# Performance work log

Hardware: AMD Instinct MI355X
Metric: run time of the kernel (lower is better)

The kernel has to match this reference:

```python
import jax, jax.numpy as jnp
import numpy as np

B, S, D, H = 2, 2048, 2048, 16
HD = D // H
EPS = 1e-5


def layernorm(x, scale, shift):
    mean = jnp.mean(x, axis=-1, keepdims=True)
    var = jnp.mean((x - mean) ** 2, axis=-1, keepdims=True)  # unbiased=False
    return scale * (x - mean) / jnp.sqrt(var + EPS) + shift


def gelu_buggy(x):
    # Faithful to source: tanh is applied ONLY to the constant sqrt(2/pi)
    c = jnp.tanh(jnp.sqrt(jnp.asarray(2.0 / jnp.pi, dtype=x.dtype)))
    return 0.5 * x * (1.0 + c * (x + 0.044715 * x ** 3))


def setup_inputs() -> dict:
    key = jax.random.key(0)
    ks = jax.random.split(key, 10)
    sd = 0.02
    return {
        "x": jax.random.normal(ks[0], (B, S, D), dtype=jnp.float32),
        "wq": jax.random.normal(ks[1], (D, D), dtype=jnp.float32) * sd,
        "wk": jax.random.normal(ks[2], (D, D), dtype=jnp.float32) * sd,
        "wv": jax.random.normal(ks[3], (D, D), dtype=jnp.float32) * sd,
        "wo": jax.random.normal(ks[4], (D, D), dtype=jnp.float32) * sd,
        "bo": jnp.zeros((D,), dtype=jnp.float32),
        "w1": jax.random.normal(ks[5], (D, 4 * D), dtype=jnp.float32) * sd,
        "b1": jnp.zeros((4 * D,), dtype=jnp.float32),
        "w2": jax.random.normal(ks[6], (4 * D, D), dtype=jnp.float32) * sd,
        "b2": jnp.zeros((D,), dtype=jnp.float32),
        "ln_scale": jnp.ones((D,), dtype=jnp.float32),
        "ln_shift": jnp.zeros((D,), dtype=jnp.float32),
    }


def attention(h, wq, wk, wv, wo, bo):
    b, s, _ = h.shape
    q = (h @ wq).reshape(b, s, H, HD).transpose(0, 2, 1, 3)  # [b,h,s,hd]
    k = (h @ wk).reshape(b, s, H, HD).transpose(0, 2, 1, 3)
    v = (h @ wv).reshape(b, s, H, HD).transpose(0, 2, 1, 3)
    scores = jnp.einsum('bhqd,bhkd->bhqk', q, k)
    causal = jnp.tril(jnp.ones((s, s), dtype=bool))
    scores = jnp.where(causal, scores, -jnp.inf)
    w = jax.nn.softmax(scores / jnp.sqrt(jnp.asarray(HD, dtype=h.dtype)), axis=-1)
    ctx = jnp.einsum('bhqk,bhkd->bhqd', w, v).transpose(0, 2, 1, 3).reshape(b, s, D)
    return ctx @ wo + bo


def reference(x, wq, wk, wv, wo, bo, w1, b1, w2, b2, ln_scale, ln_shift):
    # NB: source applies ln1 before BOTH sub-blocks (ln2 unused); dropout is identity (p=0 / eval)
    shortcut = x
    h = layernorm(x, ln_scale, ln_shift)
    h = attention(h, wq, wk, wv, wo, bo)
    x = h + shortcut
    shortcut = x
    h = layernorm(x, ln_scale, ln_shift)
    h = gelu_buggy(h @ w1 + b1) @ w2 + b2
    return h + shortcut
```

## Files before the change

kernel.cpp:

```cpp
#include <hip/hip_runtime.h>
#include <hip/hip_bf16.h>
#include <math.h>


typedef short bf16x8 __attribute__((ext_vector_type(8)));
typedef float f32x4 __attribute__((ext_vector_type(4)));
typedef short short4v __attribute__((ext_vector_type(4)));

#define MFMA16x32(a, b, c) __builtin_amdgcn_mfma_f32_16x16x32_bf16((a), (b), (c), 0, 0, 0)

__device__ __forceinline__ short f2bs(float f) {
    unsigned u = __builtin_bit_cast(unsigned, f);
    unsigned r = (u + 0x7FFFu + ((u >> 16) & 1u)) >> 16;
    return (short)(unsigned short)r;
}

__device__ __forceinline__ void gload_lds16(const void* g, void* l) {
    __builtin_amdgcn_global_load_lds(
        (const __attribute__((address_space(1))) unsigned int*)g,
        (__attribute__((address_space(3))) unsigned int*)l, 16, 0, 0);
}

template <int N>
__device__ __forceinline__ void vmw() {
    if constexpr (N == 0) asm volatile("s_waitcnt vmcnt(0)" ::: "memory");
    else if constexpr (N == 6) asm volatile("s_waitcnt vmcnt(6)" ::: "memory");
    else if constexpr (N == 8) asm volatile("s_waitcnt vmcnt(8)" ::: "memory");
    else if constexpr (N == 12) asm volatile("s_waitcnt vmcnt(12)" ::: "memory");
}

__global__ __launch_bounds__(256) void transpose_kernel(const float* __restrict__ in,
                                                        short* __restrict__ out,
                                                        int R, int C) {
    __shared__ float tile[32][33];
    const int tx = threadIdx.x & 31;
    const int ty = threadIdx.x >> 5;
    const int c0 = blockIdx.x * 32;
    const int r0 = blockIdx.y * 32;
#pragma unroll
    for (int i = 0; i < 4; ++i) {
        int r = ty + i * 8;
        tile[r][tx] = in[(size_t)(r0 + r) * C + c0 + tx];
    }
    __syncthreads();
#pragma unroll
    for (int i = 0; i < 4; ++i) {
        int r = ty + i * 8;
        out[(size_t)(c0 + r) * R + r0 + tx] = f2bs(tile[tx][r]);
    }
}

__global__ __launch_bounds__(256) void ln_kernel(const float* __restrict__ x,
                                                 const float* __restrict__ sc,
                                                 const float* __restrict__ sh,
                                                 short* __restrict__ out) {
    const int D = 2048;
    const int row = blockIdx.x;
    const int tid = threadIdx.x;
    __shared__ float red[4];
    const float4* xr = (const float4*)(x + (size_t)row * D);
    float4 v0 = xr[tid];
    float4 v1 = xr[tid + 256];
    float vals0[4] = {v0.x, v0.y, v0.z, v0.w};
    float vals1[4] = {v1.x, v1.y, v1.z, v1.w};

    float s = vals0[0] + vals0[1] + vals0[2] + vals0[3] + vals1[0] + vals1[1] + vals1[2] + vals1[3];
#pragma unroll
    for (int off = 32; off; off >>= 1) s += __shfl_xor(s, off);
    if ((tid & 63) == 0) red[tid >> 6] = s;
    __syncthreads();
    float mean = (red[0] + red[1] + red[2] + red[3]) * (1.0f / 2048.0f);
    __syncthreads();

    float q = 0.0f;
#pragma unroll
    for (int j = 0; j < 4; ++j) {
        float t0 = vals0[j] - mean;
        float t1 = vals1[j] - mean;
        q += t0 * t0 + t1 * t1;
    }
#pragma unroll
    for (int off = 32; off; off >>= 1) q += __shfl_xor(q, off);
    if ((tid & 63) == 0) red[tid >> 6] = q;
    __syncthreads();
    float var = (red[0] + red[1] + red[2] + red[3]) * (1.0f / 2048.0f);
    float inv = rsqrtf(var + 1e-5f);

    const int c0 = tid * 4;
    const int c1 = (tid + 256) * 4;
    short4v o0, o1;
#pragma unroll
    for (int j = 0; j < 4; ++j) {
        o0[j] = f2bs(sc[c0 + j] * ((vals0[j] - mean) * inv) + sh[c0 + j]);
        o1[j] = f2bs(sc[c1 + j] * ((vals1[j] - mean) * inv) + sh[c1 + j]);
    }
    *(short4v*)(out + (size_t)row * D + c0) = o0;
    *(short4v*)(out + (size_t)row * D + c1) = o1;
}

template <int EPI, int SK>
__global__ __launch_bounds__(512, 2) void gemm256(const short* __restrict__ Aop,
                                                  const short* __restrict__ Bt,
                                                  int M, int N, int K,
                                                  void* __restrict__ Cout,
                                                  float* __restrict__ part,
                                                  const float* __restrict__ bias,
                                                  const float* __restrict__ res,
                                                  float gconst) {
    constexpr int TSZ = 256 * 64;
    extern __shared__ __align__(16) short lds[];
    const int tid = threadIdx.x;
    const int lane = tid & 63;
    const int wid = tid >> 6;
    const int wm = wid >> 2, wn = wid & 3;
    const int l15 = lane & 15, grp = lane >> 4;

    const int gx = gridDim.x;
    int flat = (int)blockIdx.y * gx + (int)blockIdx.x;
    const int cpx = (gx * (int)gridDim.y) >> 3;
    flat = (flat & 7) * cpx + (flat >> 3);
    const int bx = flat % gx;
    const int byy = flat / gx;
    const int mtiles = M >> 8;
    const int myb = byy % mtiles;
    const int ksl = byy / mtiles;
    const long m0 = (long)myb * 256, n0 = (long)bx * 256;
    const int KS = K / SK;
    const long kbase = (long)ksl * KS;
    const int nt = KS >> 6;

    f32x4 zero = {0.f, 0.f, 0.f, 0.f};
    f32x4 acc[8][4];
#pragma unroll
    for (int i = 0; i < 8; i++)
#pragma unroll
        for (int j = 0; j < 4; j++) acc[i][j] = zero;

    auto STAGE = [&](int t, short* bufA, short* bufB) {
        const long k0 = kbase + ((long)t << 6);
#pragma unroll
        for (int j = 0; j < 4; ++j) {
            int c = tid + j * 512;
            int row = c >> 3, sl = (c & 7) ^ (row & 7);
            gload_lds16(Aop + (size_t)(m0 + row) * K + k0 + sl * 8, bufA + (size_t)c * 8);
        }
#pragma unroll
        for (int j = 0; j < 4; ++j) {
            int c = tid + j * 512;
            int row = c >> 3, sl = (c & 7) ^ (row & 7);
            gload_lds16(Bt + (size_t)(n0 + row) * K + k0 + sl * 8, bufB + (size_t)c * 8);
        }
    };

    STAGE(0, lds, lds + 2 * TSZ);
    STAGE(1, lds + TSZ, lds + 3 * TSZ);

    for (int t = 0; t < nt; ++t) {
        if (t == nt - 1) { vmw<0>(); } else { vmw<8>(); }
        __builtin_amdgcn_s_barrier();
        __builtin_amdgcn_sched_barrier(0);
        const short* bufA = lds + (t & 1) * TSZ;
        const short* bufB = lds + 2 * TSZ + (t & 1) * TSZ;
        __builtin_amdgcn_s_setprio(1);
#pragma unroll
        for (int kk = 0; kk < 2; ++kk) {
            bf16x8 af[8], bfr[4];
#pragma unroll
            for (int mi = 0; mi < 8; ++mi) {
                int row = wm * 128 + mi * 16 + l15;
                af[mi] = *(const bf16x8*)(bufA + row * 64 + (((kk * 4 + grp) ^ (row & 7)) * 8));
            }
#pragma unroll
            for (int ni = 0; ni < 4; ++ni) {
                int row = wn * 64 + ni * 16 + l15;
                bfr[ni] = *(const bf16x8*)(bufB + row * 64 + (((kk * 4 + grp) ^ (row & 7)) * 8));
            }
#pragma unroll
            for (int mi = 0; mi < 8; ++mi)
#pragma unroll
                for (int ni = 0; ni < 4; ++ni)
                    acc[mi][ni] = MFMA16x32(af[mi], bfr[ni], acc[mi][ni]);
        }
        __builtin_amdgcn_s_setprio(0);
        asm volatile("s_waitcnt lgkmcnt(0)" ::: "memory");
        __builtin_amdgcn_sched_barrier(0);
        __builtin_amdgcn_s_barrier();
        if (t + 2 < nt) STAGE(t + 2, lds + (t & 1) * TSZ, lds + 2 * TSZ + (t & 1) * TSZ);
    }

#pragma unroll
    for (int mi = 0; mi < 8; mi++) {
        long gr = m0 + wm * 128 + mi * 16 + grp * 4;
#pragma unroll
        for (int ni = 0; ni < 4; ni++) {
            long gcol = n0 + wn * 64 + ni * 16 + l15;
#pragma unroll
            for (int r = 0; r < 4; r++) {
                float vv = acc[mi][ni][r];
                long idx = (gr + r) * N + gcol;
                if constexpr (SK == 2) {
                    if (ksl == 1) part[idx] = vv;
                    else ((float*)Cout)[idx] = vv + bias[gcol] + res[idx];
                } else if constexpr (EPI == 0) {
                    ((short*)Cout)[idx] = f2bs(vv);
                } else {
                    float tv = vv + bias[gcol];
                    float g = 0.5f * tv * (1.0f + gconst * (tv + 0.044715f * tv * tv * tv));
                    ((short*)Cout)[idx] = f2bs(g);
                }
            }
        }
    }
}

template <int EPI>
__global__ __launch_bounds__(512, 1) void gemm3d(const short* __restrict__ A,
                                                 const short* __restrict__ Bt,
                                                 int M, int N, int K,
                                                 void* __restrict__ Cout,
                                                 const float* __restrict__ bias,
                                                 const float* __restrict__ res,
                                                 float gconst) {
    extern __shared__ __align__(16) short lds[];
    const int tid = threadIdx.x;
    const int lane = tid & 63;
    const int wid = tid >> 6;
    const int wm = wid >> 1, wn = wid & 1;
    const int l15 = lane & 15, grp = lane >> 4;

    const int gx = gridDim.x;
    int flat = (int)blockIdx.y * gx + (int)blockIdx.x;
    const int cpx = (gx * (int)gridDim.y) >> 3;
    flat = (flat & 7) * cpx + (flat >> 3);
    const int bx = flat % gx, by = flat / gx;
    const long m0 = (long)by * 256, n0 = (long)bx * 128;

    f32x4 zero = {0.f, 0.f, 0.f, 0.f};
    f32x4 acc[4][4];
#pragma unroll
    for (int i = 0; i < 4; i++)
#pragma unroll
        for (int j = 0; j < 4; j++) acc[i][j] = zero;

    auto STAGE = [&](long k0, int b) {
        short* bufA = lds + b * 24576;
        short* bufB = bufA + 16384;
#pragma unroll
        for (int j = 0; j < 4; ++j) {
            int c = tid + j * 512;
            int row = c >> 3, sl = (c & 7) ^ (row & 7);
            gload_lds16(A + (size_t)(m0 + row) * K + k0 + sl * 8,
                        bufA + (size_t)(wid * 64 + j * 512) * 8);
        }
#pragma unroll
        for (int j = 0; j < 2; ++j) {
            int c = tid + j * 512;
            int row = c >> 3, sl = (c & 7) ^ (row & 7);
            gload_lds16(Bt + (size_t)(n0 + row) * K + k0 + sl * 8,
                        bufB + (size_t)(wid * 64 + j * 512) * 8);
        }
    };

    const int nt = K >> 6;
    STAGE(0, 0);
    STAGE(64, 1);
    int cur = 0, nx2 = 2;

    for (int t = 0; t < nt; ++t) {
        if (t + 2 < nt) {
            STAGE((long)(t + 2) * 64, nx2);
            vmw<12>();
        } else if (t + 1 < nt) {
            vmw<6>();
        } else {
            vmw<0>();
        }
        __builtin_amdgcn_s_barrier();
        __builtin_amdgcn_sched_barrier(0);

        const short* bufA = lds + cur * 24576;
        const short* bufB = bufA + 16384;
        bf16x8 af[2][4], bfr[2][4];
#pragma unroll
        for (int kk = 0; kk < 2; ++kk) {
#pragma unroll
            for (int m = 0; m < 4; ++m) {
                int row = wm * 64 + m * 16 + l15;
                af[kk][m] = *(const bf16x8*)(bufA + row * 64 + (((kk * 4 + grp) ^ (row & 7)) * 8));
            }
#pragma unroll
            for (int n = 0; n < 4; ++n) {
                int row = wn * 64 + n * 16 + l15;
                bfr[kk][n] = *(const bf16x8*)(bufB + row * 64 + (((kk * 4 + grp) ^ (row & 7)) * 8));
            }
        }
        __builtin_amdgcn_s_setprio(1);
#pragma unroll
        for (int kk = 0; kk < 2; ++kk)
#pragma unroll
            for (int m = 0; m < 4; ++m)
#pragma unroll
                for (int n = 0; n < 4; ++n)
                    acc[m][n] = MFMA16x32(af[kk][m], bfr[kk][n], acc[m][n]);
        __builtin_amdgcn_s_setprio(0);
        asm volatile("s_waitcnt lgkmcnt(0)" ::: "memory");
        __builtin_amdgcn_s_barrier();
        __builtin_amdgcn_sched_barrier(0);
        cur = (cur == 2) ? 0 : cur + 1;
        nx2 = (nx2 == 2) ? 0 : nx2 + 1;
    }

#pragma unroll
    for (int m = 0; m < 4; m++) {
        long gr = m0 + wm * 64 + m * 16 + grp * 4;
#pragma unroll
        for (int n = 0; n < 4; n++) {
            long gcol = n0 + wn * 64 + n * 16 + l15;
#pragma unroll
            for (int r = 0; r < 4; r++) {
                float vv = acc[m][n][r];
                long idx = (gr + r) * N + gcol;
                if (EPI == 0) {
                    ((short*)Cout)[idx] = f2bs(vv);
                } else if (EPI == 1) {
                    ((float*)Cout)[idx] = vv + bias[gcol] + res[idx];
                } else {
                    float t2 = vv + bias[gcol];
                    float g = 0.5f * t2 * (1.0f + gconst * (t2 + 0.044715f * t2 * t2 * t2));
                    ((short*)Cout)[idx] = f2bs(g);
                }
            }
        }
    }
}

__global__ __launch_bounds__(256) void add_kernel(float* __restrict__ out,
                                                  const float* __restrict__ part,
                                                  int n4) {
    int i = blockIdx.x * 256 + threadIdx.x;
    int stride = gridDim.x * 256;
    for (; i < n4; i += stride) {
        float4 a = ((const float4*)out)[i];
        float4 b = ((const float4*)part)[i];
        a.x += b.x; a.y += b.y; a.z += b.z; a.w += b.w;
        ((float4*)out)[i] = a;
    }
}

__global__ __launch_bounds__(256) void reshape_k_kernel(const short* __restrict__ qkv,
                                                        short* __restrict__ Kh) {
    size_t idx = ((size_t)blockIdx.x * 256 + threadIdx.x) * 8;
    int d = (int)(idx & 127);
    int s = (int)((idx >> 7) & 2047);
    int bh = (int)(idx >> 18);
    int b = bh >> 4, h = bh & 15;
    const short* src = qkv + (size_t)(b * 2048 + s) * 6144 + 2048 + h * 128 + d;
    *(bf16x8*)(Kh + idx) = *(const bf16x8*)src;
}

__global__ __launch_bounds__(256) void reshape_v_kernel(const short* __restrict__ qkv,
                                                        short* __restrict__ Vt) {
    __shared__ short tile[32][33];
    const int bid = blockIdx.x;
    const int dt = bid & 3, st = (bid >> 2) & 63, bh = bid >> 8;
    const int b = bh >> 4, h = bh & 15;
    const int s0 = st * 32, d0 = dt * 32;
    const int tx = threadIdx.x & 31, ty = threadIdx.x >> 5;
#pragma unroll
    for (int i = 0; i < 4; ++i) {
        int s = ty + i * 8;
        tile[s][tx] = qkv[(size_t)(b * 2048 + s0 + s) * 6144 + 4096 + h * 128 + d0 + tx];
    }
    __syncthreads();
#pragma unroll
    for (int i = 0; i < 4; ++i) {
        int d = ty + i * 8;
        Vt[((size_t)bh * 128 + d0 + d) * 2048 + s0 + tx] = tile[tx][d];
    }
}

__global__ __launch_bounds__(256) void flash3_kernel(const short* __restrict__ qp,
                                                     const short* __restrict__ Kh,
                                                     const short* __restrict__ Vt,
                                                     short* __restrict__ ctx) {
    const int S = 2048, D = 2048, HD = 128, LD = 6144;
    __shared__ __align__(16) short Ks[2][64 * 128];
    __shared__ __align__(16) short Vs[2][64 * 128];
    __shared__ __align__(16) short Ps[4][16 * 64];
    const int tid = threadIdx.x;
    const int lane = tid & 63, wid = tid >> 6;
    const int l15 = lane & 15, grp = lane >> 4;

    int bid = (int)blockIdx.x;
    bid = (bid & 7) * 64 + (bid >> 3);
    const int p = bid & 15, bh = bid >> 4;
    const int b = bh >> 4, h = bh & 15;
    const int qtH = 31 - p;
    const int nH = qtH + 1;
    const float scale = 0.08838834764831845f;
    const float NEGINF = -__builtin_inff();

    const short* Kbase = Kh + (size_t)bh * S * 128;
    const short* Vbase = Vt + (size_t)bh * 128 * S;
    short* Psw = &Ps[wid][0];

    f32x4 zero = {0.f, 0.f, 0.f, 0.f};
    bf16x8 aq[4];
    float m_[4], l_[4];
    f32x4 o[8];

    int qt = qtH;
    int qw = qt * 64 + wid * 16;
    {
        const short* qrow = qp + (size_t)(b * S + qw + l15) * LD + h * HD;
#pragma unroll
        for (int kc = 0; kc < 4; kc++) aq[kc] = *(const bf16x8*)(qrow + kc * 32 + grp * 8);
    }
#pragma unroll
    for (int r = 0; r < 4; r++) { m_[r] = NEGINF; l_[r] = 0.f; }
#pragma unroll
    for (int n = 0; n < 8; n++) o[n] = zero;

#pragma unroll
    for (int j = 0; j < 4; ++j) {
        int c = tid + j * 256;
        int r = c >> 4, sl = c & 15;
        gload_lds16(Kbase + (size_t)r * 128 + ((sl ^ (r & 7)) * 8),
                    Ks[0] + (size_t)(wid * 64 + j * 256) * 8);
    }
#pragma unroll
    for (int j = 0; j < 4; ++j) {
        int c = tid + j * 256;
        int d = c >> 3, sl = c & 7;
        gload_lds16(Vbase + (size_t)d * S + ((sl ^ (d & 7)) * 8),
                    Vs[0] + (size_t)(wid * 64 + j * 256) * 8);
    }
    __syncthreads();

    int cur = 0;
    for (int i = 0; i < 33; ++i) {
        const int kt = (i < nH) ? i : (i - nH);
        const bool lastT = (kt == qt);

        if (i + 1 < 33) {
            const int ktn = (i + 1 < nH) ? (i + 1) : (i + 1 - nH);
            const long kn0 = (long)ktn * 64;
            const short* Kg = Kbase + kn0 * 128;
            const short* Vg = Vbase + kn0;
            short* kd = Ks[cur ^ 1];
            short* vd = Vs[cur ^ 1];
#pragma unroll
            for (int j = 0; j < 4; ++j) {
                int c = tid + j * 256;
                int r = c >> 4, sl = c & 15;
                gload_lds16(Kg + (size_t)r * 128 + ((sl ^ (r & 7)) * 8),
                            kd + (size_t)(wid * 64 + j * 256) * 8);
            }
#pragma unroll
            for (int j = 0; j < 4; ++j) {
                int c = tid + j * 256;
                int d = c >> 3, sl = c & 7;
                gload_lds16(Vg + (size_t)d * S + ((sl ^ (d & 7)) * 8),
                            vd + (size_t)(wid * 64 + j * 256) * 8);
            }
        }

        const short* Kc = Ks[cur];
        const short* Vc = Vs[cur];

        f32x4 s[4] = {zero, zero, zero, zero};
#pragma unroll
        for (int n = 0; n < 4; ++n) {
            int r = n * 16 + l15;
#pragma unroll
            for (int kc = 0; kc < 4; ++kc) {
                bf16x8 kb = *(const bf16x8*)(Kc + r * 128 + (((kc * 4 + grp) ^ (r & 7)) * 8));
                s[n] = MFMA16x32(aq[kc], kb, s[n]);
            }
        }

        float al[4];
#pragma unroll
        for (int r = 0; r < 4; ++r) {
            float v[4];
#pragma unroll
            for (int n = 0; n < 4; ++n) v[n] = s[n][r] * scale;
            if (lastT) {
                int qrel = wid * 16 + grp * 4 + r;
#pragma unroll
                for (int n = 0; n < 4; ++n)
                    if (n * 16 + l15 > qrel) v[n] = NEGINF;
            }
            float mx = fmaxf(fmaxf(v[0], v[1]), fmaxf(v[2], v[3]));
            mx = fmaxf(mx, __shfl_xor(mx, 1));
            mx = fmaxf(mx, __shfl_xor(mx, 2));
            mx = fmaxf(mx, __shfl_xor(mx, 4));
            mx = fmaxf(mx, __shfl_xor(mx, 8));
            float mn = fmaxf(m_[r], mx);
            float sc_ = __expf(m_[r] - mn);
            float rs = 0.f;
            int q = grp * 4 + r;
#pragma unroll
            for (int n = 0; n < 4; ++n) {
                v[n] = __expf(v[n] - mn);
                rs += v[n];
                Psw[q * 64 + (((n * 2 + (l15 >> 3)) ^ (q & 7)) * 8) + (l15 & 7)] = f2bs(v[n]);
            }
            rs += __shfl_xor(rs, 1);
            rs += __shfl_xor(rs, 2);
            rs += __shfl_xor(rs, 4);
            rs += __shfl_xor(rs, 8);
            l_[r] = l_[r] * sc_ + rs;
            m_[r] = mn;
            al[r] = sc_;
        }
#pragma unroll
        for (int n = 0; n < 8; n++) {
            f32x4 t = o[n];
            t[0] *= al[0]; t[1] *= al[1]; t[2] *= al[2]; t[3] *= al[3];
            o[n] = t;
        }

        bf16x8 pa[2];
#pragma unroll
        for (int kc = 0; kc < 2; ++kc)
            pa[kc] = *(const bf16x8*)(Psw + l15 * 64 + (((kc * 4 + grp) ^ (l15 & 7)) * 8));
#pragma unroll
        for (int n = 0; n < 8; ++n) {
            int d = n * 16 + l15;
#pragma unroll
            for (int kc = 0; kc < 2; ++kc) {
                bf16x8 vb = *(const bf16x8*)(Vc + d * 64 + (((kc * 4 + grp) ^ (d & 7)) * 8));
                o[n] = MFMA16x32(pa[kc], vb, o[n]);
            }
        }

        if (lastT) {
            float inv[4];
#pragma unroll
            for (int r = 0; r < 4; ++r) inv[r] = 1.0f / l_[r];
            short* cb_ = ctx + (size_t)(b * S + qw + grp * 4) * D + h * HD + l15;
#pragma unroll
            for (int n = 0; n < 8; ++n)
#pragma unroll
                for (int r = 0; r < 4; ++r)
                    cb_[(size_t)r * D + n * 16] = f2bs(o[n][r] * inv[r]);
            if (i < 32) {
                qt = 31 - qtH;
                qw = qt * 64 + wid * 16;
                const short* qrow = qp + (size_t)(b * S + qw + l15) * LD + h * HD;
#pragma unroll
                for (int kc = 0; kc < 4; kc++) aq[kc] = *(const bf16x8*)(qrow + kc * 32 + grp * 8);
#pragma unroll
                for (int r = 0; r < 4; r++) { m_[r] = NEGINF; l_[r] = 0.f; }
#pragma unroll
                for (int n = 0; n < 8; n++) o[n] = zero;
            }
        }
        __syncthreads();
        cur ^= 1;
    }
}

extern "C" void kernel_launch(void* const* d_in, const int* in_sizes, int n_in,
                              void* d_out, int out_size, void* d_ws, size_t ws_size,
                              hipStream_t stream) {
    const float* x    = (const float*)d_in[0];
    const float* wq   = (const float*)d_in[1];
    const float* wk   = (const float*)d_in[2];
    const float* wv   = (const float*)d_in[3];
    const float* wo   = (const float*)d_in[4];
    const float* bo   = (const float*)d_in[5];
    const float* w1   = (const float*)d_in[6];
    const float* b1   = (const float*)d_in[7];
    const float* w2   = (const float*)d_in[8];
    const float* b2   = (const float*)d_in[9];
    const float* lnsc = (const float*)d_in[10];
    const float* lnsh = (const float*)d_in[11];

    const int B = 2, S = 2048, D = 2048;
    const int M = B * S;
    const int LDS_256 = 4 * 256 * 64 * 2;
    const int LDS_3D  = 3 * 24576 * 2;

    char* p = (char*)d_ws;
    short* wqkvT = (short*)p; p += (size_t)3 * D * D * 2;
    short* woT   = (short*)p; p += (size_t)D * D * 2;
    short* w1T   = (short*)p; p += (size_t)4 * D * D * 2;
    short* w2T   = (short*)p; p += (size_t)4 * D * D * 2;
    short* lnb   = (short*)p; p += (size_t)M * D * 2;
    short* qkvb  = (short*)p;
    short* h1    = qkvb;
    p += (size_t)M * 3 * D * 2;
    short* ctxb  = (short*)p; p += (size_t)M * D * 2;
    float* x2    = (float*)p; p += (size_t)M * D * 4;

    short* Kh = wqkvT;
    short* Vt = (short*)x2;
    float* part = (float*)d_ws;

    const float gconst = tanhf(sqrtf(2.0f / 3.14159265358979323846f));

    hipFuncSetAttribute((const void*)&gemm256<0, 1>, hipFuncAttributeMaxDynamicSharedMemorySize, LDS_256);
    hipFuncSetAttribute((const void*)&gemm256<2, 1>, hipFuncAttributeMaxDynamicSharedMemorySize, LDS_256);
    hipFuncSetAttribute((const void*)&gemm256<1, 2>, hipFuncAttributeMaxDynamicSharedMemorySize, LDS_256);
    hipFuncSetAttribute((const void*)&gemm3d<1>, hipFuncAttributeMaxDynamicSharedMemorySize, LDS_3D);

    dim3 blk(256);
    transpose_kernel<<<dim3(64, 64), blk, 0, stream>>>(wq, wqkvT, D, D);
    transpose_kernel<<<dim3(64, 64), blk, 0, stream>>>(wk, wqkvT + (size_t)D * D, D, D);
    transpose_kernel<<<dim3(64, 64), blk, 0, stream>>>(wv, wqkvT + (size_t)2 * D * D, D, D);
    transpose_kernel<<<dim3(64, 64), blk, 0, stream>>>(wo, woT, D, D);
    transpose_kernel<<<dim3(256, 64), blk, 0, stream>>>(w1, w1T, D, 4 * D);
    transpose_kernel<<<dim3(64, 256), blk, 0, stream>>>(w2, w2T, 4 * D, D);

    ln_kernel<<<dim3(M), blk, 0, stream>>>(x, lnsc, lnsh, lnb);
    gemm256<0, 1><<<dim3(3 * D / 256, M / 256), dim3(512), LDS_256, stream>>>(
        lnb, wqkvT, M, 3 * D, D, qkvb, nullptr, nullptr, nullptr, 0.f);

    reshape_k_kernel<<<dim3(4096), blk, 0, stream>>>(qkvb, Kh);
    reshape_v_kernel<<<dim3(8192), blk, 0, stream>>>(qkvb, Vt);

    flash3_kernel<<<dim3(512), blk, 0, stream>>>(qkvb, Kh, Vt, ctxb);

    gemm3d<1><<<dim3(D / 128, M / 256), dim3(512), LDS_3D, stream>>>(
        ctxb, woT, M, D, D, x2, bo, x, 0.f);
    ln_kernel<<<dim3(M), blk, 0, stream>>>(x2, lnsc, lnsh, lnb);
    gemm256<2, 1><<<dim3(4 * D / 256, M / 256), dim3(512), LDS_256, stream>>>(
        lnb, w1T, M, 4 * D, D, h1, nullptr, b1, nullptr, gconst);
    gemm256<1, 2><<<dim3(D / 256, 2 * M / 256), dim3(512), LDS_256, stream>>>(
        h1, w2T, M, D, 4 * D, (float*)d_out, part, b2, x2, 0.f);
    add_kernel<<<dim3(2048), blk, 0, stream>>>((float*)d_out, part, M * D / 4);
}
```

Baseline: 666.4 us.

## Drop split-K and K reshape; read K directly from QKV buffer

Removes the split-K path from the 256-tile GEMM and its follow-up add kernel, and runs the FFN down-projection with the 128-wide gemm3d kernel using a fused bias+residual epilogue. The QKV projection also switches to gemm3d. The K reshape kernel is removed, and flash attention loads K tiles straight from the strided QKV buffer. This cuts one extra kernel launch, one partial-sum round trip and one K copy, but the down-projection loses split-K parallelism and K loads now use a strided row pitch.

After: 627.5 us. 1.06x faster.

```diff
diff --git a/kernel.cpp b/kernel.cpp
--- a/kernel.cpp
+++ b/kernel.cpp
@@ -98,12 +98,11 @@
     *(short4v*)(out + (size_t)row * D + c1) = o1;
 }
 
-template <int EPI, int SK>
+template <int EPI>
 __global__ __launch_bounds__(512, 2) void gemm256(const short* __restrict__ Aop,
                                                   const short* __restrict__ Bt,
                                                   int M, int N, int K,
                                                   void* __restrict__ Cout,
-                                                  float* __restrict__ part,
                                                   const float* __restrict__ bias,
                                                   const float* __restrict__ res,
                                                   float gconst) {
@@ -119,15 +118,9 @@
     int flat = (int)blockIdx.y * gx + (int)blockIdx.x;
     const int cpx = (gx * (int)gridDim.y) >> 3;
     flat = (flat & 7) * cpx + (flat >> 3);
-    const int bx = flat % gx;
-    const int byy = flat / gx;
-    const int mtiles = M >> 8;
-    const int myb = byy % mtiles;
-    const int ksl = byy / mtiles;
-    const long m0 = (long)myb * 256, n0 = (long)bx * 256;
-    const int KS = K / SK;
-    const long kbase = (long)ksl * KS;
-    const int nt = KS >> 6;
+    const int bx = flat % gx, by = flat / gx;
+    const long m0 = (long)by * 256, n0 = (long)bx * 256;
+    const int nt = K >> 6;
 
     f32x4 zero = {0.f, 0.f, 0.f, 0.f};
     f32x4 acc[8][4];
@@ -137,7 +130,7 @@
         for (int j = 0; j < 4; j++) acc[i][j] = zero;
 
     auto STAGE = [&](int t, short* bufA, short* bufB) {
-        const long k0 = kbase + ((long)t << 6);
+        const long k0 = (long)t << 6;
 #pragma unroll
         for (int j = 0; j < 4; ++j) {
             int c = tid + j * 512;
@@ -198,11 +191,10 @@
             for (int r = 0; r < 4; r++) {
                 float vv = acc[mi][ni][r];
                 long idx = (gr + r) * N + gcol;
-                if constexpr (SK == 2) {
-                    if (ksl == 1) part[idx] = vv;
-                    else ((float*)Cout)[idx] = vv + bias[gcol] + res[idx];
-                } else if constexpr (EPI == 0) {
+                if constexpr (EPI == 0) {
                     ((short*)Cout)[idx] = f2bs(vv);
+                } else if constexpr (EPI == 1) {
+                    ((float*)Cout)[idx] = vv + bias[gcol] + res[idx];
                 } else {
                     float tv = vv + bias[gcol];
                     float g = 0.5f * tv * (1.0f + gconst * (tv + 0.044715f * tv * tv * tv));
@@ -334,30 +326,6 @@
     }
 }
 
-__global__ __launch_bounds__(256) void add_kernel(float* __restrict__ out,
-                                                  const float* __restrict__ part,
-                                                  int n4) {
-    int i = blockIdx.x * 256 + threadIdx.x;
-    int stride = gridDim.x * 256;
-    for (; i < n4; i += stride) {
-        float4 a = ((const float4*)out)[i];
-        float4 b = ((const float4*)part)[i];
-        a.x += b.x; a.y += b.y; a.z += b.z; a.w += b.w;
-        ((float4*)out)[i] = a;
-    }
-}
-
-__global__ __launch_bounds__(256) void reshape_k_kernel(const short* __restrict__ qkv,
-                                                        short* __restrict__ Kh) {
-    size_t idx = ((size_t)blockIdx.x * 256 + threadIdx.x) * 8;
-    int d = (int)(idx & 127);
-    int s = (int)((idx >> 7) & 2047);
-    int bh = (int)(idx >> 18);
-    int b = bh >> 4, h = bh & 15;
-    const short* src = qkv + (size_t)(b * 2048 + s) * 6144 + 2048 + h * 128 + d;
-    *(bf16x8*)(Kh + idx) = *(const bf16x8*)src;
-}
-
 __global__ __launch_bounds__(256) void reshape_v_kernel(const short* __restrict__ qkv,
                                                         short* __restrict__ Vt) {
     __shared__ short tile[32][33];
@@ -380,7 +348,6 @@
 }
 
 __global__ __launch_bounds__(256) void flash3_kernel(const short* __restrict__ qp,
-                                                     const short* __restrict__ Kh,
                                                      const short* __restrict__ Vt,
                                                      short* __restrict__ ctx) {
     const int S = 2048, D = 2048, HD = 128, LD = 6144;
@@ -400,7 +367,7 @@
     const float scale = 0.08838834764831845f;
     const float NEGINF = -__builtin_inff();
 
-    const short* Kbase = Kh + (size_t)bh * S * 128;
+    const short* Kbase = qp + (size_t)b * S * LD + 2048 + (size_t)h * HD;
     const short* Vbase = Vt + (size_t)bh * 128 * S;
     short* Psw = &Ps[wid][0];
 
@@ -425,7 +392,7 @@
     for (int j = 0; j < 4; ++j) {
         int c = tid + j * 256;
         int r = c >> 4, sl = c & 15;
-        gload_lds16(Kbase + (size_t)r * 128 + ((sl ^ (r & 7)) * 8),
+        gload_lds16(Kbase + (size_t)r * LD + ((sl ^ (r & 7)) * 8),
                     Ks[0] + (size_t)(wid * 64 + j * 256) * 8);
     }
 #pragma unroll
@@ -445,7 +412,7 @@
         if (i + 1 < 33) {
             const int ktn = (i + 1 < nH) ? (i + 1) : (i + 1 - nH);
             const long kn0 = (long)ktn * 64;
-            const short* Kg = Kbase + kn0 * 128;
+            const short* Kg = Kbase + (size_t)kn0 * LD;
             const short* Vg = Vbase + kn0;
             short* kd = Ks[cur ^ 1];
             short* vd = Vs[cur ^ 1];
@@ -453,7 +420,7 @@
             for (int j = 0; j < 4; ++j) {
                 int c = tid + j * 256;
                 int r = c >> 4, sl = c & 15;
-                gload_lds16(Kg + (size_t)r * 128 + ((sl ^ (r & 7)) * 8),
+                gload_lds16(Kg + (size_t)r * LD + ((sl ^ (r & 7)) * 8),
                             kd + (size_t)(wid * 64 + j * 256) * 8);
             }
 #pragma unroll
@@ -595,15 +562,12 @@
     short* ctxb  = (short*)p; p += (size_t)M * D * 2;
     float* x2    = (float*)p; p += (size_t)M * D * 4;
 
-    short* Kh = wqkvT;
     short* Vt = (short*)x2;
-    float* part = (float*)d_ws;
 
     const float gconst = tanhf(sqrtf(2.0f / 3.14159265358979323846f));
 
-    hipFuncSetAttribute((const void*)&gemm256<0, 1>, hipFuncAttributeMaxDynamicSharedMemorySize, LDS_256);
-    hipFuncSetAttribute((const void*)&gemm256<2, 1>, hipFuncAttributeMaxDynamicSharedMemorySize, LDS_256);
-    hipFuncSetAttribute((const void*)&gemm256<1, 2>, hipFuncAttributeMaxDynamicSharedMemorySize, LDS_256);
+    hipFuncSetAttribute((const void*)&gemm256<2>, hipFuncAttributeMaxDynamicSharedMemorySize, LDS_256);
+    hipFuncSetAttribute((const void*)&gemm3d<0>, hipFuncAttributeMaxDynamicSharedMemorySize, LDS_3D);
     hipFuncSetAttribute((const void*)&gemm3d<1>, hipFuncAttributeMaxDynamicSharedMemorySize, LDS_3D);
 
     dim3 blk(256);
@@ -615,20 +579,18 @@
     transpose_kernel<<<dim3(64, 256), blk, 0, stream>>>(w2, w2T, 4 * D, D);
 
     ln_kernel<<<dim3(M), blk, 0, stream>>>(x, lnsc, lnsh, lnb);
-    gemm256<0, 1><<<dim3(3 * D / 256, M / 256), dim3(512), LDS_256, stream>>>(
-        lnb, wqkvT, M, 3 * D, D, qkvb, nullptr, nullptr, nullptr, 0.f);
-
-    reshape_k_kernel<<<dim3(4096), blk, 0, stream>>>(qkvb, Kh);
+    gemm3d<0><<<dim3(3 * D / 128, M / 256), dim3(512), LDS_3D, stream>>>(
+        lnb, wqkvT, M, 3 * D, D, qkvb, nullptr, nullptr, 0.f);
+
     reshape_v_kernel<<<dim3(8192), blk, 0, stream>>>(qkvb, Vt);
 
-    flash3_kernel<<<dim3(512), blk, 0, stream>>>(qkvb, Kh, Vt, ctxb);
+    flash3_kernel<<<dim3(512), blk, 0, stream>>>(qkvb, Vt, ctxb);
 
     gemm3d<1><<<dim3(D / 128, M / 256), dim3(512), LDS_3D, stream>>>(
         ctxb, woT, M, D, D, x2, bo, x, 0.f);
     ln_kernel<<<dim3(M), blk, 0, stream>>>(x2, lnsc, lnsh, lnb);
-    gemm256<2, 1><<<dim3(4 * D / 256, M / 256), dim3(512), LDS_256, stream>>>(
-        lnb, w1T, M, 4 * D, D, h1, nullptr, b1, nullptr, gconst);
-    gemm256<1, 2><<<dim3(D / 256, 2 * M / 256), dim3(512), LDS_256, stream>>>(
-        h1, w2T, M, D, 4 * D, (float*)d_out, part, b2, x2, 0.f);
-    add_kernel<<<dim3(2048), blk, 0, stream>>>((float*)d_out, part, M * D / 4);
-}
+    gemm256<2><<<dim3(4 * D / 256, M / 256), dim3(512), LDS_256, stream>>>(
+        lnb, w1T, M, 4 * D, D, h1, b1, nullptr, gconst);
+    gemm3d<1><<<dim3(D / 128, M / 256), dim3(512), LDS_3D, stream>>>(
+        h1, w2T, M, D, 4 * D, (float*)d_out, b2, x2, 0.f);
+}
```
